# Kernel optimization log

Hardware: AMD Instinct MI355X
Metric: run time of the kernel (lower is better)

Reference implementation:

```python
import jax, jax.numpy as jnp
import numpy as np

T, B, H, O = 1024, 256, 512, 64  # target_len, batch, hidden_size, output_size


def setup_inputs() -> dict:
    key = jax.random.key(0)
    ks = jax.random.split(key, 8)
    s_ih = 1.0 / np.sqrt(H)
    return {
        "code_vec": jax.random.normal(ks[0], (1, B, H), dtype=jnp.float32),
        "target": jax.random.normal(ks[1], (T, B, O), dtype=jnp.float32),
        "w_ih": jax.random.normal(ks[2], (3 * H, O), dtype=jnp.float32) * s_ih,
        "w_hh": jax.random.normal(ks[3], (3 * H, H), dtype=jnp.float32) * s_ih,
        "b_ih": jax.random.normal(ks[4], (3 * H,), dtype=jnp.float32) * s_ih,
        "b_hh": jax.random.normal(ks[5], (3 * H,), dtype=jnp.float32) * s_ih,
        "w_out": jax.random.normal(ks[6], (O, H), dtype=jnp.float32) * s_ih,
        "b_out": jax.random.normal(ks[7], (O,), dtype=jnp.float32) * s_ih,
    }


def reference(code_vec, target, w_ih, w_hh, b_ih, b_hh, w_out, b_out):
    # Teacher-forced GRU decoder: input at t=0 is zeros, then target[t-1].
    xs = jnp.concatenate([jnp.zeros((1, B, O), target.dtype), target[:-1]], axis=0)
    h0 = code_vec[0]  # [B, H] (n_layers == 1)

    def step(h, x):
        gi = x @ w_ih.T + b_ih            # [B, 3H]
        gh = h @ w_hh.T + b_hh            # [B, 3H]
        i_r, i_z, i_n = jnp.split(gi, 3, axis=-1)
        h_r, h_z, h_n = jnp.split(gh, 3, axis=-1)
        r = jax.nn.sigmoid(i_r + h_r)
        z = jax.nn.sigmoid(i_z + h_z)
        n = jnp.tanh(i_n + r * h_n)
        h_new = (1.0 - z) * n + z * h
        y = h_new @ w_out.T + b_out       # [B, O]
        return h_new, y

    h_last, outputs = jax.lax.scan(step, h0, xs)
    return outputs, h_last[None]  # ([T,B,O], [1,B,H])
```

## Files before the change

### kernel.cpp

```cpp
#include <hip/hip_runtime.h>

#define TSTEPS 1024
#define BATCH  256
#define HID    512
#define OUTD   64

#define NWG    256
#define NTHR   256
#define UPW    16
#define KPAD   68

__device__ __forceinline__ float red8(float v) {
  v += __shfl_xor(v, 1);
  v += __shfl_xor(v, 2);
  v += __shfl_xor(v, 4);
  return v;
}

__device__ __forceinline__ float sigmoidf_(float x) {
  float t = __expf(-fabsf(x));
  float p = 1.f / (1.f + t);
  return x >= 0.f ? p : 1.f - p;
}

__device__ __forceinline__ float tanhf_(float x) {
  float t = __expf(-2.f * fabsf(x));
  float p = (1.f - t) / (1.f + t);
  return x >= 0.f ? p : -p;
}

__global__ void __launch_bounds__(NTHR, 1)
gru_step(const float* __restrict__ target,
         const float* __restrict__ w_ih,
         const float* __restrict__ w_hh,
         const float* __restrict__ b_ih,
         const float* __restrict__ b_hh,
         const float* __restrict__ w_out,
         const float* __restrict__ b_out,
         const float* __restrict__ hread,
         float* __restrict__ hwrite,
         float* __restrict__ out,
         int s)
{
  __shared__ float whh_s [3*UPW*8*KPAD];
  __shared__ float wih_s [3*UPW*64];
  __shared__ float wout_s[2*8*KPAD];
  __shared__ float bih_s [48];
  __shared__ float bhh_s [48];
  __shared__ float bout_s[2];

  const int bid = blockIdx.x;
  const int g   = bid >> 5;
  const int cu  = bid & 31;
  const int tid = threadIdx.x;
  const int ln  = tid & 63;
  const int bl  = ((tid >> 6) << 3) | (ln >> 3);
  const int bg  = (g << 5) | bl;
  const int ks  = ln & 7;

  for (int i = tid; i < 48*HID; i += NTHR) {
    int c = i >> 9, k = i & 511;
    int grow = (c >> 4)*HID + cu*UPW + (c & 15);
    whh_s[(c*8 + (k >> 6))*KPAD + (k & 63)] = w_hh[grow*HID + k];
  }
  for (int i = tid; i < 48*64; i += NTHR) {
    int c = i >> 6, k = i & 63;
    int grow = (c >> 4)*HID + cu*UPW + (c & 15);
    wih_s[i] = w_ih[grow*OUTD + k];
  }
  for (int i = tid; i < 2*HID; i += NTHR) {
    int o2 = i >> 9, k = i & 511;
    wout_s[(o2*8 + (k >> 6))*KPAD + (k & 63)] = w_out[(cu*2 + o2)*HID + k];
  }
  if (tid < 48) {
    int grow = (tid >> 4)*HID + cu*UPW + (tid & 15);
    bih_s[tid] = b_ih[grow];
    bhh_s[tid] = b_hh[grow];
  }
  if (tid < 2) bout_s[tid] = b_out[cu*2 + tid];
  __syncthreads();

  const float* hsrc = hread + (size_t)bg*HID;
  float hreg[64];
  #pragma unroll
  for (int j = 0; j < 64; j += 4) {
    float4 v = *reinterpret_cast<const float4*>(hsrc + ks*64 + j);
    hreg[j+0]=v.x; hreg[j+1]=v.y; hreg[j+2]=v.z; hreg[j+3]=v.w;
  }
  float hown[UPW];
  #pragma unroll
  for (int j = 0; j < UPW; j += 4) {
    float4 v = *reinterpret_cast<const float4*>(hsrc + cu*UPW + j);
    hown[j+0]=v.x; hown[j+1]=v.y; hown[j+2]=v.z; hown[j+3]=v.w;
  }
  float xreg[8];
  if (s > 0) {
    const float* xp = target + ((size_t)(s-1)*BATCH + bg)*OUTD + ks*8;
    float4 a = *reinterpret_cast<const float4*>(xp);
    float4 b = *reinterpret_cast<const float4*>(xp + 4);
    xreg[0]=a.x; xreg[1]=a.y; xreg[2]=a.z; xreg[3]=a.w;
    xreg[4]=b.x; xreg[5]=b.y; xreg[6]=b.z; xreg[7]=b.w;
  } else {
    #pragma unroll
    for (int j = 0; j < 8; ++j) xreg[j] = 0.f;
  }

  if (s > 0) {
    #pragma unroll
    for (int o2 = 0; o2 < 2; ++o2) {
      const float* row = wout_s + (o2*8 + ks)*KPAD;
      float acc = 0.f;
      #pragma unroll
      for (int j = 0; j < 64; ++j) acc = fmaf(hreg[j], row[j], acc);
      acc = red8(acc);
      if (ks == 0)
        out[((size_t)(s-1)*BATCH + bg)*OUTD + (cu*2 + o2)] = acc + bout_s[o2];
    }
  }

  float hnew[UPW];
  #pragma unroll
  for (int u = 0; u < UPW; ++u) {
    const float* rr = whh_s + ((0*UPW + u)*8 + ks)*KPAD;
    const float* rz = whh_s + ((1*UPW + u)*8 + ks)*KPAD;
    const float* rn = whh_s + ((2*UPW + u)*8 + ks)*KPAD;
    float ghr = 0.f, ghz = 0.f, ghn = 0.f;
    #pragma unroll
    for (int j = 0; j < 64; ++j) {
      ghr = fmaf(hreg[j], rr[j], ghr);
      ghz = fmaf(hreg[j], rz[j], ghz);
      ghn = fmaf(hreg[j], rn[j], ghn);
    }
    const float* ir_ = wih_s + (0*UPW + u)*64 + ks*8;
    const float* iz_ = wih_s + (1*UPW + u)*64 + ks*8;
    const float* in_ = wih_s + (2*UPW + u)*64 + ks*8;
    float gir = 0.f, giz = 0.f, gin = 0.f;
    #pragma unroll
    for (int j = 0; j < 8; ++j) {
      gir = fmaf(xreg[j], ir_[j], gir);
      giz = fmaf(xreg[j], iz_[j], giz);
      gin = fmaf(xreg[j], in_[j], gin);
    }
    float sr  = red8(ghr + gir);
    float sz  = red8(ghz + giz);
    float sni = red8(gin);
    float snh = red8(ghn);
    float r = sigmoidf_(sr + bih_s[u]      + bhh_s[u]);
    float z = sigmoidf_(sz + bih_s[16 + u] + bhh_s[16 + u]);
    float n = tanhf_((sni + bih_s[32 + u]) + r*(snh + bhh_s[32 + u]));
    hnew[u] = (1.f - z)*n + z*hown[u];
  }

  float* hdst = hwrite + (size_t)bg*HID + cu*UPW;
  if (ks == 0) {
    #pragma unroll
    for (int j = 0; j < UPW; j += 4)
      *reinterpret_cast<float4*>(hdst + j) =
          make_float4(hnew[j], hnew[j+1], hnew[j+2], hnew[j+3]);
  }
}

__global__ void __launch_bounds__(NTHR, 1)
gru_tail(const float* __restrict__ w_out,
         const float* __restrict__ b_out,
         const float* __restrict__ hlast,
         float* __restrict__ out)
{
  __shared__ float wout_s[2*8*KPAD];
  __shared__ float bout_s[2];

  const int bid = blockIdx.x;
  const int g   = bid >> 5;
  const int cu  = bid & 31;
  const int tid = threadIdx.x;
  const int ln  = tid & 63;
  const int bl  = ((tid >> 6) << 3) | (ln >> 3);
  const int bg  = (g << 5) | bl;
  const int ks  = ln & 7;

  for (int i = tid; i < 2*HID; i += NTHR) {
    int o2 = i >> 9, k = i & 511;
    wout_s[(o2*8 + (k >> 6))*KPAD + (k & 63)] = w_out[(cu*2 + o2)*HID + k];
  }
  if (tid < 2) bout_s[tid] = b_out[cu*2 + tid];
  __syncthreads();

  const float* hsrc = hlast + (size_t)bg*HID;
  float hreg[64];
  #pragma unroll
  for (int j = 0; j < 64; j += 4) {
    float4 v = *reinterpret_cast<const float4*>(hsrc + ks*64 + j);
    hreg[j+0]=v.x; hreg[j+1]=v.y; hreg[j+2]=v.z; hreg[j+3]=v.w;
  }
  #pragma unroll
  for (int o2 = 0; o2 < 2; ++o2) {
    const float* row = wout_s + (o2*8 + ks)*KPAD;
    float acc = 0.f;
    #pragma unroll
    for (int j = 0; j < 64; ++j) acc = fmaf(hreg[j], row[j], acc);
    acc = red8(acc);
    if (ks == 0)
      out[((size_t)(TSTEPS-1)*BATCH + bg)*OUTD + (cu*2 + o2)] = acc + bout_s[o2];
  }
}

extern "C" void kernel_launch(void* const* d_in, const int* in_sizes, int n_in,
                              void* d_out, int out_size, void* d_ws, size_t ws_size,
                              hipStream_t stream) {
  const float* code_vec = (const float*)d_in[0];
  const float* target   = (const float*)d_in[1];
  const float* w_ih     = (const float*)d_in[2];
  const float* w_hh     = (const float*)d_in[3];
  const float* b_ih     = (const float*)d_in[4];
  const float* b_hh     = (const float*)d_in[5];
  const float* w_out    = (const float*)d_in[6];
  const float* b_out    = (const float*)d_in[7];
  float* out = (float*)d_out;
  float* h0  = (float*)d_ws;
  float* h1  = h0 + (size_t)BATCH*HID;

  for (int s = 0; s < TSTEPS; ++s) {
    const float* hread = (s == 0) ? code_vec : ((s & 1) ? h0 : h1);
    float* hwrite      = (s & 1) ? h1 : h0;
    gru_step<<<NWG, NTHR, 0, stream>>>(target, w_ih, w_hh, b_ih, b_hh,
                                       w_out, b_out, hread, hwrite, out, s);
  }
  gru_tail<<<NWG, NTHR, 0, stream>>>(w_out, b_out, h1, out);
  hipMemcpyAsync(out + (size_t)TSTEPS*BATCH*OUTD, h1,
                 (size_t)BATCH*HID*sizeof(float),
                 hipMemcpyDeviceToDevice, stream);
}
```

Before: 38.77 ms.

## Fuse per-step GRU launches into one persistent kernel with per-group barriers

Replaces 1024 per-timestep kernel launches plus a tail kernel with one persistent kernel. Each workgroup loads its weights into shared memory once and loops over time steps. Workgroups that share a batch group synchronise through an atomic counter spin barrier, and the block-to-(group, unit) mapping is changed so each barrier spans only 32 workgroups. This removes launch overhead and the per-step weight reload into LDS. In exchange it depends on all 256 workgroups being co-resident, and the spin barriers add latency and deadlock risk if they are not.

```diff
diff --git a/kernel.cpp b/kernel.cpp
--- a/kernel.cpp
+++ b/kernel.cpp
@@ -30,17 +30,17 @@
 }
 
 __global__ void __launch_bounds__(NTHR, 1)
-gru_step(const float* __restrict__ target,
-         const float* __restrict__ w_ih,
-         const float* __restrict__ w_hh,
-         const float* __restrict__ b_ih,
-         const float* __restrict__ b_hh,
-         const float* __restrict__ w_out,
-         const float* __restrict__ b_out,
-         const float* __restrict__ hread,
-         float* __restrict__ hwrite,
-         float* __restrict__ out,
-         int s)
+gru_persist(const float* __restrict__ code_vec,
+            const float* __restrict__ target,
+            const float* __restrict__ w_ih,
+            const float* __restrict__ w_hh,
+            const float* __restrict__ b_ih,
+            const float* __restrict__ b_hh,
+            const float* __restrict__ w_out,
+            const float* __restrict__ b_out,
+            float* __restrict__ out,
+            float* __restrict__ ws,
+            int*   __restrict__ cnt)
 {
   __shared__ float whh_s [3*UPW*8*KPAD];
   __shared__ float wih_s [3*UPW*64];
@@ -50,8 +50,8 @@
   __shared__ float bout_s[2];
 
   const int bid = blockIdx.x;
-  const int g   = bid >> 5;
-  const int cu  = bid & 31;
+  const int g   = bid & 7;
+  const int cu  = bid >> 3;
   const int tid = threadIdx.x;
   const int ln  = tid & 63;
   const int bl  = ((tid >> 6) << 3) | (ln >> 3);
@@ -80,32 +80,113 @@
   if (tid < 2) bout_s[tid] = b_out[cu*2 + tid];
   __syncthreads();
 
-  const float* hsrc = hread + (size_t)bg*HID;
-  float hreg[64];
+  float* hbuf0 = ws;
+  float* hbuf1 = ws + BATCH*HID;
+
+  float xreg[8];
   #pragma unroll
-  for (int j = 0; j < 64; j += 4) {
-    float4 v = *reinterpret_cast<const float4*>(hsrc + ks*64 + j);
-    hreg[j+0]=v.x; hreg[j+1]=v.y; hreg[j+2]=v.z; hreg[j+3]=v.w;
-  }
-  float hown[UPW];
-  #pragma unroll
-  for (int j = 0; j < UPW; j += 4) {
-    float4 v = *reinterpret_cast<const float4*>(hsrc + cu*UPW + j);
-    hown[j+0]=v.x; hown[j+1]=v.y; hown[j+2]=v.z; hown[j+3]=v.w;
-  }
-  float xreg[8];
-  if (s > 0) {
-    const float* xp = target + ((size_t)(s-1)*BATCH + bg)*OUTD + ks*8;
-    float4 a = *reinterpret_cast<const float4*>(xp);
-    float4 b = *reinterpret_cast<const float4*>(xp + 4);
-    xreg[0]=a.x; xreg[1]=a.y; xreg[2]=a.z; xreg[3]=a.w;
-    xreg[4]=b.x; xreg[5]=b.y; xreg[6]=b.z; xreg[7]=b.w;
-  } else {
-    #pragma unroll
-    for (int j = 0; j < 8; ++j) xreg[j] = 0.f;
-  }
-
-  if (s > 0) {
+  for (int j = 0; j < 8; ++j) xreg[j] = 0.f;
+
+  for (int s = 0; s < TSTEPS; ++s) {
+    const float* hsrc = (s == 0) ? (code_vec + (size_t)bg*HID)
+                                 : (((s & 1) ? hbuf0 : hbuf1) + (size_t)bg*HID);
+    float hreg[64];
+    #pragma unroll
+    for (int j = 0; j < 64; j += 4) {
+      float4 v = *reinterpret_cast<const float4*>(hsrc + ks*64 + j);
+      hreg[j+0]=v.x; hreg[j+1]=v.y; hreg[j+2]=v.z; hreg[j+3]=v.w;
+    }
+    float hown[UPW];
+    #pragma unroll
+    for (int j = 0; j < UPW; j += 4) {
+      float4 v = *reinterpret_cast<const float4*>(hsrc + cu*UPW + j);
+      hown[j+0]=v.x; hown[j+1]=v.y; hown[j+2]=v.z; hown[j+3]=v.w;
+    }
+
+    if (s > 0) {
+      #pragma unroll
+      for (int o2 = 0; o2 < 2; ++o2) {
+        const float* row = wout_s + (o2*8 + ks)*KPAD;
+        float acc = 0.f;
+        #pragma unroll
+        for (int j = 0; j < 64; ++j) acc = fmaf(hreg[j], row[j], acc);
+        acc = red8(acc);
+        if (ks == 0)
+          out[((size_t)(s-1)*BATCH + bg)*OUTD + (cu*2 + o2)] = acc + bout_s[o2];
+      }
+    }
+
+    float hnew[UPW];
+    #pragma unroll
+    for (int u = 0; u < UPW; ++u) {
+      const float* rr = whh_s + ((0*UPW + u)*8 + ks)*KPAD;
+      const float* rz = whh_s + ((1*UPW + u)*8 + ks)*KPAD;
+      const float* rn = whh_s + ((2*UPW + u)*8 + ks)*KPAD;
+      float ghr = 0.f, ghz = 0.f, ghn = 0.f;
+      #pragma unroll
+      for (int j = 0; j < 64; ++j) {
+        ghr = fmaf(hreg[j], rr[j], ghr);
+        ghz = fmaf(hreg[j], rz[j], ghz);
+        ghn = fmaf(hreg[j], rn[j], ghn);
+      }
+      const float* ir_ = wih_s + (0*UPW + u)*64 + ks*8;
+      const float* iz_ = wih_s + (1*UPW + u)*64 + ks*8;
+      const float* in_ = wih_s + (2*UPW + u)*64 + ks*8;
+      float gir = 0.f, giz = 0.f, gin = 0.f;
+      #pragma unroll
+      for (int j = 0; j < 8; ++j) {
+        gir = fmaf(xreg[j], ir_[j], gir);
+        giz = fmaf(xreg[j], iz_[j], giz);
+        gin = fmaf(xreg[j], in_[j], gin);
+      }
+      float sr  = red8(ghr + gir);
+      float sz  = red8(ghz + giz);
+      float sni = red8(gin);
+      float snh = red8(ghn);
+      float r = sigmoidf_(sr + bih_s[u]      + bhh_s[u]);
+      float z = sigmoidf_(sz + bih_s[16 + u] + bhh_s[16 + u]);
+      float n = tanhf_((sni + bih_s[32 + u]) + r*(snh + bhh_s[32 + u]));
+      hnew[u] = (1.f - z)*n + z*hown[u];
+    }
+
+    float* hdst = ((s & 1) ? hbuf1 : hbuf0) + (size_t)bg*HID + cu*UPW;
+    if (ks == 0) {
+      #pragma unroll
+      for (int j = 0; j < UPW; j += 4)
+        *reinterpret_cast<float4*>(hdst + j) =
+            make_float4(hnew[j], hnew[j+1], hnew[j+2], hnew[j+3]);
+    }
+
+    __syncthreads();
+    if (tid == 0) {
+      __threadfence();
+      atomicAdd(&cnt[g], 1);
+    }
+    if (s + 1 < TSTEPS) {
+      const float* xp = target + ((size_t)s*BATCH + bg)*OUTD + ks*8;
+      float4 a = *reinterpret_cast<const float4*>(xp);
+      float4 b = *reinterpret_cast<const float4*>(xp + 4);
+      xreg[0]=a.x; xreg[1]=a.y; xreg[2]=a.z; xreg[3]=a.w;
+      xreg[4]=b.x; xreg[5]=b.y; xreg[6]=b.z; xreg[7]=b.w;
+    }
+    if (tid == 0) {
+      const int want = 32*(s + 1);
+      while (__hip_atomic_load(&cnt[g], __ATOMIC_ACQUIRE,
+                               __HIP_MEMORY_SCOPE_AGENT) < want)
+        __builtin_amdgcn_s_sleep(1);
+    }
+    __syncthreads();
+    __threadfence();
+  }
+
+  {
+    const float* hsrc = hbuf1 + (size_t)bg*HID;
+    float hreg[64];
+    #pragma unroll
+    for (int j = 0; j < 64; j += 4) {
+      float4 v = *reinterpret_cast<const float4*>(hsrc + ks*64 + j);
+      hreg[j+0]=v.x; hreg[j+1]=v.y; hreg[j+2]=v.z; hreg[j+3]=v.w;
+    }
     #pragma unroll
     for (int o2 = 0; o2 < 2; ++o2) {
       const float* row = wout_s + (o2*8 + ks)*KPAD;
@@ -114,93 +195,8 @@
       for (int j = 0; j < 64; ++j) acc = fmaf(hreg[j], row[j], acc);
       acc = red8(acc);
       if (ks == 0)
-        out[((size_t)(s-1)*BATCH + bg)*OUTD + (cu*2 + o2)] = acc + bout_s[o2];
-    }
-  }
-
-  float hnew[UPW];
-  #pragma unroll
-  for (int u = 0; u < UPW; ++u) {
-    const float* rr = whh_s + ((0*UPW + u)*8 + ks)*KPAD;
-    const float* rz = whh_s + ((1*UPW + u)*8 + ks)*KPAD;
-    const float* rn = whh_s + ((2*UPW + u)*8 + ks)*KPAD;
-    float ghr = 0.f, ghz = 0.f, ghn = 0.f;
-    #pragma unroll
-    for (int j = 0; j < 64; ++j) {
-      ghr = fmaf(hreg[j], rr[j], ghr);
-      ghz = fmaf(hreg[j], rz[j], ghz);
-      ghn = fmaf(hreg[j], rn[j], ghn);
-    }
-    const float* ir_ = wih_s + (0*UPW + u)*64 + ks*8;
-    const float* iz_ = wih_s + (1*UPW + u)*64 + ks*8;
-    const float* in_ = wih_s + (2*UPW + u)*64 + ks*8;
-    float gir = 0.f, giz = 0.f, gin = 0.f;
-    #pragma unroll
-    for (int j = 0; j < 8; ++j) {
-      gir = fmaf(xreg[j], ir_[j], gir);
-      giz = fmaf(xreg[j], iz_[j], giz);
-      gin = fmaf(xreg[j], in_[j], gin);
-    }
-    float sr  = red8(ghr + gir);
-    float sz  = red8(ghz + giz);
-    float sni = red8(gin);
-    float snh = red8(ghn);
-    float r = sigmoidf_(sr + bih_s[u]      + bhh_s[u]);
-    float z = sigmoidf_(sz + bih_s[16 + u] + bhh_s[16 + u]);
-    float n = tanhf_((sni + bih_s[32 + u]) + r*(snh + bhh_s[32 + u]));
-    hnew[u] = (1.f - z)*n + z*hown[u];
-  }
-
-  float* hdst = hwrite + (size_t)bg*HID + cu*UPW;
-  if (ks == 0) {
-    #pragma unroll
-    for (int j = 0; j < UPW; j += 4)
-      *reinterpret_cast<float4*>(hdst + j) =
-          make_float4(hnew[j], hnew[j+1], hnew[j+2], hnew[j+3]);
-  }
-}
-
-__global__ void __launch_bounds__(NTHR, 1)
-gru_tail(const float* __restrict__ w_out,
-         const float* __restrict__ b_out,
-         const float* __restrict__ hlast,
-         float* __restrict__ out)
-{
-  __shared__ float wout_s[2*8*KPAD];
-  __shared__ float bout_s[2];
-
-  const int bid = blockIdx.x;
-  const int g   = bid >> 5;
-  const int cu  = bid & 31;
-  const int tid = threadIdx.x;
-  const int ln  = tid & 63;
-  const int bl  = ((tid >> 6) << 3) | (ln >> 3);
-  const int bg  = (g << 5) | bl;
-  const int ks  = ln & 7;
-
-  for (int i = tid; i < 2*HID; i += NTHR) {
-    int o2 = i >> 9, k = i & 511;
-    wout_s[(o2*8 + (k >> 6))*KPAD + (k & 63)] = w_out[(cu*2 + o2)*HID + k];
-  }
-  if (tid < 2) bout_s[tid] = b_out[cu*2 + tid];
-  __syncthreads();
-
-  const float* hsrc = hlast + (size_t)bg*HID;
-  float hreg[64];
-  #pragma unroll
-  for (int j = 0; j < 64; j += 4) {
-    float4 v = *reinterpret_cast<const float4*>(hsrc + ks*64 + j);
-    hreg[j+0]=v.x; hreg[j+1]=v.y; hreg[j+2]=v.z; hreg[j+3]=v.w;
-  }
-  #pragma unroll
-  for (int o2 = 0; o2 < 2; ++o2) {
-    const float* row = wout_s + (o2*8 + ks)*KPAD;
-    float acc = 0.f;
-    #pragma unroll
-    for (int j = 0; j < 64; ++j) acc = fmaf(hreg[j], row[j], acc);
-    acc = red8(acc);
-    if (ks == 0)
-      out[((size_t)(TSTEPS-1)*BATCH + bg)*OUTD + (cu*2 + o2)] = acc + bout_s[o2];
+        out[((size_t)(TSTEPS-1)*BATCH + bg)*OUTD + (cu*2 + o2)] = acc + bout_s[o2];
+    }
   }
 }
 
@@ -216,16 +212,16 @@
   const float* w_out    = (const float*)d_in[6];
   const float* b_out    = (const float*)d_in[7];
   float* out = (float*)d_out;
-  float* h0  = (float*)d_ws;
-  float* h1  = h0 + (size_t)BATCH*HID;
-
-  for (int s = 0; s < TSTEPS; ++s) {
-    const float* hread = (s == 0) ? code_vec : ((s & 1) ? h0 : h1);
-    float* hwrite      = (s & 1) ? h1 : h0;
-    gru_step<<<NWG, NTHR, 0, stream>>>(target, w_ih, w_hh, b_ih, b_hh,
-                                       w_out, b_out, hread, hwrite, out, s);
-  }
-  gru_tail<<<NWG, NTHR, 0, stream>>>(w_out, b_out, h1, out);
+  float* ws  = (float*)d_ws;
+  float* h1  = ws + (size_t)BATCH*HID;
+  int*   cnt = (int*)(ws + (size_t)2*BATCH*HID);
+
+  hipMemsetAsync(cnt, 0, 8*sizeof(int), stream);
+
+  gru_persist<<<NWG, NTHR, 0, stream>>>(code_vec, target, w_ih, w_hh,
+                                        b_ih, b_hh, w_out, b_out,
+                                        out, ws, cnt);
+
   hipMemcpyAsync(out + (size_t)TSTEPS*BATCH*OUTD, h1,
                  (size_t)BATCH*HID*sizeof(float),
                  hipMemcpyDeviceToDevice, stream);
```

New measurement: 102.2 ms. +163.6%, slower.
